# Optimization experiments

Measured on AMD Instinct MI355X. Metric: run time of the kernel, lower is better.

The kernel has to match this reference:

```python
import jax, jax.numpy as jnp
import numpy as np

ALPHA = 2.0  # init kwarg alpha


def _edt(mask):
    """Exact Euclidean distance from each pixel to the nearest False pixel.
    mask: (H, W) bool. Matches scipy.ndimage.distance_transform_edt(mask).
    Separable algorithm: 1D L1 pass along columns, then exact min over columns.
    """
    H, W = mask.shape
    INF = jnp.float32(H + W)
    g0 = jnp.where(mask, INF, 0.0).astype(jnp.float32)  # 0 at background pixels

    def step(carry, row):
        g = jnp.minimum(row, carry + 1.0)
        return g, g

    _, fwd = jax.lax.scan(step, jnp.full((W,), INF, jnp.float32), g0)
    _, bwd = jax.lax.scan(step, jnp.full((W,), INF, jnp.float32), fwd[::-1])
    g = bwd[::-1]  # (H, W): vertical distance to nearest bg in same column

    j = jnp.arange(W, dtype=jnp.float32)
    d2 = (j[:, None] - j[None, :]) ** 2  # (Wj, Wk)
    # dist2[i, j] = min_k g[i, k]^2 + (j - k)^2   -> exact squared EDT
    dist2 = jnp.min(g[:, None, :] ** 2 + d2[None, :, :], axis=-1)  # (H, W)
    return jnp.sqrt(dist2)


def _distance_field(img):
    """img: (N, H, W) float. Replicates LogHausdorffDTLoss.distance_field per slice."""

    def one(ch):
        mask = ch > 0.5
        valid = jnp.logical_and(mask.any(), ~mask.all())
        field = _edt(mask) + _edt(~mask)  # fg_dist + bg_dist
        return jnp.where(valid, field, 0.0)

    # sequential map keeps peak memory to one (H, W, W) intermediate at a time
    return jax.lax.map(one, img)


def setup_inputs() -> dict:
    key = jax.random.key(0)
    k1, k2, k3 = jax.random.split(key, 3)
    B, C, H, W = 8, 4, 256, 256
    preds_S = jax.random.normal(k1, (B, C, H, W), dtype=jnp.float32)
    preds_T = jax.random.normal(k2, (B, C, H, W), dtype=jnp.float32)
    target = jax.random.uniform(k3, (B, 1, H, W), dtype=jnp.float32)
    return {"preds_S": preds_S, "preds_T": preds_T, "target": target}


def reference(preds_S, preds_T, target):
    # shapes already match -> no interpolation; sigmoid=False, softmax=True, C>1
    C = preds_S.shape[1]
    p = jax.nn.softmax(preds_S, axis=1)

    # to_onehot_y=True: target is overwritten by onehot(argmax(teacher)) (detached)
    pT = jax.lax.stop_gradient(preds_T)
    labels = jnp.argmax(pT, axis=1)  # (B, H, W)
    tgt = jax.nn.one_hot(labels, C, axis=1, dtype=p.dtype)  # (B, C, H, W)

    # include_background=False: drop channel 0
    p = p[:, 1:]
    tgt = tgt[:, 1:]
    B, Cc, H, W = p.shape

    pred_dt = _distance_field(jax.lax.stop_gradient(p).reshape(-1, H, W)).reshape(B, Cc, H, W)
    tgt_dt = _distance_field(tgt.reshape(-1, H, W)).reshape(B, Cc, H, W)
    pred_dt = jax.lax.stop_gradient(pred_dt)
    tgt_dt = jax.lax.stop_gradient(tgt_dt)

    err = (p - tgt) ** 2
    dist = pred_dt ** ALPHA + tgt_dt ** ALPHA
    # per-channel means all cover B*H*W elements -> mean of means == global mean
    loss = jnp.mean(err * dist)
    return jnp.log(loss + 1.0)
```

## Files before the change

### kernel.cpp

```cpp
#include <hip/hip_runtime.h>
#include <math.h>

#define HWTOT 65536
#define WD 256
#define NSL 24

static constexpr size_t OFF_PART = 256;
static constexpr size_t OFF_MASK = 24832;
static constexpr size_t OFF_ERR  = OFF_MASK + (size_t)NSL * HWTOT;
static constexpr size_t OFF_BITS = OFF_ERR + (size_t)NSL * HWTOT * 2;
static constexpr size_t OFF_GC   = OFF_BITS + (size_t)2 * NSL * 8 * WD * 4;

__global__ __launch_bounds__(256) void k_mask(
    const float* __restrict__ pS, const float* __restrict__ pT,
    unsigned char* __restrict__ mask, _Float16* __restrict__ err)
{
    int blk = blockIdx.x;
    int b   = blk >> 8;
    int hw  = (blk & 255) * 256 + threadIdx.x;

    const float* ps = pS + (size_t)b * 4 * HWTOT + hw;
    float s0 = ps[0], s1 = ps[HWTOT], s2 = ps[2 * HWTOT], s3 = ps[3 * HWTOT];
    float mx = fmaxf(fmaxf(s0, s1), fmaxf(s2, s3));
    float e0 = expf(s0 - mx), e1 = expf(s1 - mx), e2 = expf(s2 - mx), e3 = expf(s3 - mx);
    float inv = 1.0f / (e0 + e1 + e2 + e3);

    const float* pt = pT + (size_t)b * 4 * HWTOT + hw;
    float t0 = pt[0], t1 = pt[HWTOT], t2 = pt[2 * HWTOT], t3 = pt[3 * HWTOT];
    int lab = 0; float bm = t0;
    if (t1 > bm) { bm = t1; lab = 1; }
    if (t2 > bm) { bm = t2; lab = 2; }
    if (t3 > bm) { bm = t3; lab = 3; }

    float pv[3] = { e1 * inv, e2 * inv, e3 * inv };
    #pragma unroll
    for (int cc = 0; cc < 3; ++cc) {
        int sl = b * 3 + cc;
        bool mp = pv[cc] > 0.5f;
        bool mt = (lab == cc + 1);
        mask[(size_t)sl * HWTOT + hw] = (unsigned char)((mp ? 1 : 0) | (mt ? 2 : 0));
        float tcv = mt ? 1.0f : 0.0f;
        float ev = (pv[cc] - tcv) * (pv[cc] - tcv);
        err[(size_t)sl * HWTOT + hw] = (_Float16)ev;
    }
}

__global__ __launch_bounds__(256) void k_pack(
    const unsigned char* __restrict__ mask, unsigned* __restrict__ bits)
{
    int s = blockIdx.x;
    int k = blockIdx.y;
    int w = threadIdx.x;
    const unsigned char* m = mask + (size_t)s * HWTOT + k * 32 * WD + w;

    unsigned vp = 0, vt = 0;
    #pragma unroll
    for (int i = 0; i < 32; ++i) {
        unsigned v = m[i * WD];
        vp |= (v & 1u) << i;
        vt |= ((v >> 1) & 1u) << i;
    }
    bits[((size_t)(0 * NSL + s) * 8 + k) * WD + w] = vp;
    bits[((size_t)(1 * NSL + s) * 8 + k) * WD + w] = vt;
}

__device__ __forceinline__ void vgc_field(
    const unsigned Y[8], bool valid, int kk, int w,
    unsigned short* __restrict__ gout)
{
    unsigned wk = 0;
    #pragma unroll
    for (int j = 0; j < 8; ++j) if (j == kk) wk = Y[j];

    int ls = -1000, lc = -1000;
    #pragma unroll
    for (int j = 0; j < 8; ++j) {
        if (j < kk) {
            unsigned z = Y[j], zc = ~Y[j];
            ls = z  ? (32 * j + 31 - __clz(z))  : ls;
            lc = zc ? (32 * j + 31 - __clz(zc)) : lc;
        }
    }
    unsigned dupk[16];
    #pragma unroll
    for (int r = 0; r < 32; ++r) {
        int h = 32 * kk + r;
        int b = (wk >> r) & 1;
        int du = min(h - (b ? lc : ls), 512);
        if (r & 1) dupk[r >> 1] |= (unsigned)du << 16;
        else       dupk[r >> 1]  = (unsigned)du;
        ls = b ? h : ls;
        lc = b ? lc : h;
    }
    int ns = 100000, nc = 100000;
    #pragma unroll
    for (int j = 7; j >= 0; --j) {
        if (j > kk) {
            unsigned z = Y[j], zc = ~Y[j];
            ns = z  ? (32 * j + (__ffs(z)  - 1)) : ns;
            nc = zc ? (32 * j + (__ffs(zc) - 1)) : nc;
        }
    }
    #pragma unroll
    for (int r = 31; r >= 0; --r) {
        int h = 32 * kk + r;
        int b = (wk >> r) & 1;
        int dd = min((b ? nc : ns) - h, 512);
        unsigned pk = dupk[r >> 1];
        int du = (r & 1) ? (int)(pk >> 16) : (int)(pk & 0xffffu);
        int gcv = min(du, dd);
        gcv = valid ? gcv : 0;
        gout[h * WD + w] = (unsigned short)gcv;
        ns = b ? h : ns;
        nc = b ? nc : h;
    }
}

__global__ __launch_bounds__(256) void k_vgc(
    const unsigned* __restrict__ bits, unsigned short* __restrict__ gc)
{
    int s  = blockIdx.x;
    int kk = blockIdx.y;
    int w  = threadIdx.x;

    unsigned YP[8], YT[8];
    #pragma unroll
    for (int j = 0; j < 8; ++j) {
        YP[j] = bits[((size_t)(0 * NSL + s) * 8 + j) * WD + w];
        YT[j] = bits[((size_t)(1 * NSL + s) * 8 + j) * WD + w];
    }

    unsigned oP = 0, aP = 0xFFFFFFFFu, oT = 0, aT = 0xFFFFFFFFu;
    #pragma unroll
    for (int j = 0; j < 8; ++j) {
        oP |= YP[j]; aP &= YP[j];
        oT |= YT[j]; aT &= YT[j];
    }
    #pragma unroll
    for (int i = 1; i < 64; i <<= 1) {
        oP |= __shfl_xor(oP, i); aP &= __shfl_xor(aP, i);
        oT |= __shfl_xor(oT, i); aT &= __shfl_xor(aT, i);
    }
    __shared__ unsigned rb[4][4];
    if ((w & 63) == 0) {
        int wv = w >> 6;
        rb[wv][0] = oP; rb[wv][1] = aP; rb[wv][2] = oT; rb[wv][3] = aT;
    }
    __syncthreads();
    oP = rb[0][0] | rb[1][0] | rb[2][0] | rb[3][0];
    aP = rb[0][1] & rb[1][1] & rb[2][1] & rb[3][1];
    oT = rb[0][2] | rb[1][2] | rb[2][2] | rb[3][2];
    aT = rb[0][3] & rb[1][3] & rb[2][3] & rb[3][3];
    bool validP = (oP != 0u) && (aP != 0xFFFFFFFFu);
    bool validT = (oT != 0u) && (aT != 0xFFFFFFFFu);

    vgc_field(YP, validP, kk, w, gc + (size_t)(0 * NSL + s) * HWTOT);
    vgc_field(YT, validT, kk, w, gc + (size_t)(1 * NSL + s) * HWTOT);
}

__global__ __launch_bounds__(256) void k_row(
    const _Float16* __restrict__ err, const unsigned* __restrict__ bits,
    const unsigned short* __restrict__ gcArr, float* __restrict__ partials)
{
    int h  = blockIdx.x;
    int s  = blockIdx.y;
    int jo = threadIdx.x;

    __shared__ float4 g2[768];
    __shared__ float  wred[4];

    size_t rbase = (size_t)s * HWTOT + h * WD + jo;
    int gcP = gcArr[rbase];
    int gcT = gcArr[(size_t)NSL * HWTOT + rbase];
    unsigned wP = bits[((size_t)(0 * NSL + s) * 8 + (h >> 5)) * WD + jo];
    unsigned wT = bits[((size_t)(1 * NSL + s) * 8 + (h >> 5)) * WD + jo];
    bool selP = (wP >> (h & 31)) & 1;
    bool selT = (wT >> (h & 31)) & 1;

    float fP = (float)(gcP * gcP);
    float fT = (float)(gcT * gcT);
    g2[256 + jo] = make_float4(selP ? fP : 0.0f, selP ? 0.0f : fP,
                               selT ? fT : 0.0f, selT ? 0.0f : fT);
    float4 inf4 = make_float4(1e30f, 1e30f, 1e30f, 1e30f);
    g2[jo] = inf4;
    g2[512 + jo] = inf4;

    int R = min(max(gcP, gcT), 256);
    #pragma unroll
    for (int i = 1; i < 64; i <<= 1) R = max(R, __shfl_xor(R, i));

    float m1 = fP;
    float m2 = fT;
    __syncthreads();

    for (int dd = 1; dd < R; ++dd) {
        float4 L  = g2[256 + jo - dd];
        float4 Rv = g2[256 + jo + dd];
        float d2 = (float)(dd * dd);
        float c1 = fminf(selP ? L.x : L.y, selP ? Rv.x : Rv.y);
        float c2 = fminf(selT ? L.z : L.w, selT ? Rv.z : Rv.w);
        m1 = fminf(m1, c1 + d2);
        m2 = fminf(m2, c2 + d2);
    }

    float contrib = (float)err[rbase] * (m1 + m2);

    #pragma unroll
    for (int off = 32; off > 0; off >>= 1) contrib += __shfl_down(contrib, off);
    if ((jo & 63) == 0) wred[jo >> 6] = contrib;
    __syncthreads();
    if (jo == 0) partials[s * 256 + h] = wred[0] + wred[1] + wred[2] + wred[3];
}

__global__ __launch_bounds__(256) void k_final(
    const float* __restrict__ partials, float* __restrict__ out)
{
    __shared__ double red[256];
    int t = threadIdx.x;
    double acc = 0.0;
    for (int i = t; i < NSL * 256; i += 256) acc += (double)partials[i];
    red[t] = acc;
    __syncthreads();
    for (int off = 128; off > 0; off >>= 1) {
        if (t < off) red[t] += red[t + off];
        __syncthreads();
    }
    if (t == 0) {
        double loss = red[0] / (double)((size_t)NSL * HWTOT);
        out[0] = (float)log(loss + 1.0);
    }
}

extern "C" void kernel_launch(void* const* d_in, const int* in_sizes, int n_in,
                              void* d_out, int out_size, void* d_ws, size_t ws_size,
                              hipStream_t stream)
{
    const float* pS = (const float*)d_in[0];
    const float* pT = (const float*)d_in[1];
    float* out = (float*)d_out;

    char* ws = (char*)d_ws;
    float*          parts = (float*)(ws + OFF_PART);
    unsigned char*  mask  = (unsigned char*)(ws + OFF_MASK);
    _Float16*       err   = (_Float16*)(ws + OFF_ERR);
    unsigned*       bits  = (unsigned*)(ws + OFF_BITS);
    unsigned short* gc    = (unsigned short*)(ws + OFF_GC);

    k_mask <<<dim3(2048),     dim3(256), 0, stream>>>(pS, pT, mask, err);
    k_pack <<<dim3(NSL, 8),   dim3(256), 0, stream>>>(mask, bits);
    k_vgc  <<<dim3(NSL, 8),   dim3(256), 0, stream>>>(bits, gc);
    k_row  <<<dim3(256, NSL), dim3(256), 0, stream>>>(err, bits, gc, parts);
    k_final<<<dim3(1),        dim3(256), 0, stream>>>(parts, out);
}
```

Baseline: 105.4 us.

## Fuse vertical pass, row min pass and final reduction into one kernel

Merges the column-distance, per-row horizontal min and final reduction kernels into one kernel. Column distances are kept in LDS instead of written to global memory, and a last-block atomic counter performs the final log reduction. This removes two launches and the global gc round-trip. In exchange the row pass goes from 6144 blocks to 192, with each block iterating 32 rows serially under barriers, which reduces parallelism.

```diff
diff --git a/kernel.cpp b/kernel.cpp
--- a/kernel.cpp
+++ b/kernel.cpp
@@ -4,12 +4,13 @@
 #define HWTOT 65536
 #define WD 256
 #define NSL 24
-
+#define NBLK (NSL * 8)
+
+static constexpr size_t OFF_DONE = 0;
 static constexpr size_t OFF_PART = 256;
 static constexpr size_t OFF_MASK = 24832;
 static constexpr size_t OFF_ERR  = OFF_MASK + (size_t)NSL * HWTOT;
 static constexpr size_t OFF_BITS = OFF_ERR + (size_t)NSL * HWTOT * 2;
-static constexpr size_t OFF_GC   = OFF_BITS + (size_t)2 * NSL * 8 * WD * 4;
 
 __global__ __launch_bounds__(256) void k_mask(
     const float* __restrict__ pS, const float* __restrict__ pT,
@@ -46,7 +47,8 @@
 }
 
 __global__ __launch_bounds__(256) void k_pack(
-    const unsigned char* __restrict__ mask, unsigned* __restrict__ bits)
+    const unsigned char* __restrict__ mask, unsigned* __restrict__ bits,
+    unsigned* __restrict__ done)
 {
     int s = blockIdx.x;
     int k = blockIdx.y;
@@ -62,9 +64,11 @@
     }
     bits[((size_t)(0 * NSL + s) * 8 + k) * WD + w] = vp;
     bits[((size_t)(1 * NSL + s) * 8 + k) * WD + w] = vt;
-}
-
-__device__ __forceinline__ void vgc_field(
+
+    if (s == 0 && k == 0 && w == 0) *done = 0;
+}
+
+__device__ __forceinline__ void vgc_field_lds(
     const unsigned Y[8], bool valid, int kk, int w,
     unsigned short* __restrict__ gout)
 {
@@ -110,26 +114,36 @@
         int du = (r & 1) ? (int)(pk >> 16) : (int)(pk & 0xffffu);
         int gcv = min(du, dd);
         gcv = valid ? gcv : 0;
-        gout[h * WD + w] = (unsigned short)gcv;
+        gout[r * WD + w] = (unsigned short)gcv;
         ns = b ? h : ns;
         nc = b ? nc : h;
     }
 }
 
-__global__ __launch_bounds__(256) void k_vgc(
-    const unsigned* __restrict__ bits, unsigned short* __restrict__ gc)
-{
-    int s  = blockIdx.x;
-    int kk = blockIdx.y;
-    int w  = threadIdx.x;
+__global__ __launch_bounds__(256) void k_fused(
+    const _Float16* __restrict__ err, const unsigned* __restrict__ bits,
+    float* __restrict__ partials, unsigned* __restrict__ done,
+    float* __restrict__ out)
+{
+    int s   = blockIdx.x;
+    int kk  = blockIdx.y;
+    int jo  = threadIdx.x;
+    int bid = s * 8 + kk;
+
+    __shared__ float4         g2[768];
+    __shared__ unsigned short gcP_l[32 * WD];
+    __shared__ unsigned short gcT_l[32 * WD];
+    __shared__ unsigned       rb[4][4];
+    __shared__ float          wred[4];
+    __shared__ int            amLast;
+    __shared__ double         dred[256];
 
     unsigned YP[8], YT[8];
     #pragma unroll
     for (int j = 0; j < 8; ++j) {
-        YP[j] = bits[((size_t)(0 * NSL + s) * 8 + j) * WD + w];
-        YT[j] = bits[((size_t)(1 * NSL + s) * 8 + j) * WD + w];
-    }
-
+        YP[j] = bits[((size_t)(0 * NSL + s) * 8 + j) * WD + jo];
+        YT[j] = bits[((size_t)(1 * NSL + s) * 8 + j) * WD + jo];
+    }
     unsigned oP = 0, aP = 0xFFFFFFFFu, oT = 0, aT = 0xFFFFFFFFu;
     #pragma unroll
     for (int j = 0; j < 8; ++j) {
@@ -141,9 +155,8 @@
         oP |= __shfl_xor(oP, i); aP &= __shfl_xor(aP, i);
         oT |= __shfl_xor(oT, i); aT &= __shfl_xor(aT, i);
     }
-    __shared__ unsigned rb[4][4];
-    if ((w & 63) == 0) {
-        int wv = w >> 6;
+    if ((jo & 63) == 0) {
+        int wv = jo >> 6;
         rb[wv][0] = oP; rb[wv][1] = aP; rb[wv][2] = oT; rb[wv][3] = aT;
     }
     __syncthreads();
@@ -154,80 +167,80 @@
     bool validP = (oP != 0u) && (aP != 0xFFFFFFFFu);
     bool validT = (oT != 0u) && (aT != 0xFFFFFFFFu);
 
-    vgc_field(YP, validP, kk, w, gc + (size_t)(0 * NSL + s) * HWTOT);
-    vgc_field(YT, validT, kk, w, gc + (size_t)(1 * NSL + s) * HWTOT);
-}
-
-__global__ __launch_bounds__(256) void k_row(
-    const _Float16* __restrict__ err, const unsigned* __restrict__ bits,
-    const unsigned short* __restrict__ gcArr, float* __restrict__ partials)
-{
-    int h  = blockIdx.x;
-    int s  = blockIdx.y;
-    int jo = threadIdx.x;
-
-    __shared__ float4 g2[768];
-    __shared__ float  wred[4];
-
-    size_t rbase = (size_t)s * HWTOT + h * WD + jo;
-    int gcP = gcArr[rbase];
-    int gcT = gcArr[(size_t)NSL * HWTOT + rbase];
-    unsigned wP = bits[((size_t)(0 * NSL + s) * 8 + (h >> 5)) * WD + jo];
-    unsigned wT = bits[((size_t)(1 * NSL + s) * 8 + (h >> 5)) * WD + jo];
-    bool selP = (wP >> (h & 31)) & 1;
-    bool selT = (wT >> (h & 31)) & 1;
-
-    float fP = (float)(gcP * gcP);
-    float fT = (float)(gcT * gcT);
-    g2[256 + jo] = make_float4(selP ? fP : 0.0f, selP ? 0.0f : fP,
-                               selT ? fT : 0.0f, selT ? 0.0f : fT);
+    vgc_field_lds(YP, validP, kk, jo, gcP_l);
+    vgc_field_lds(YT, validT, kk, jo, gcT_l);
+
+    unsigned wkP = 0, wkT = 0;
+    #pragma unroll
+    for (int j = 0; j < 8; ++j) if (j == kk) { wkP = YP[j]; wkT = YT[j]; }
+
     float4 inf4 = make_float4(1e30f, 1e30f, 1e30f, 1e30f);
     g2[jo] = inf4;
     g2[512 + jo] = inf4;
-
-    int R = min(max(gcP, gcT), 256);
-    #pragma unroll
-    for (int i = 1; i < 64; i <<= 1) R = max(R, __shfl_xor(R, i));
-
-    float m1 = fP;
-    float m2 = fT;
-    __syncthreads();
-
-    for (int dd = 1; dd < R; ++dd) {
-        float4 L  = g2[256 + jo - dd];
-        float4 Rv = g2[256 + jo + dd];
-        float d2 = (float)(dd * dd);
-        float c1 = fminf(selP ? L.x : L.y, selP ? Rv.x : Rv.y);
-        float c2 = fminf(selT ? L.z : L.w, selT ? Rv.z : Rv.w);
-        m1 = fminf(m1, c1 + d2);
-        m2 = fminf(m2, c2 + d2);
-    }
-
-    float contrib = (float)err[rbase] * (m1 + m2);
-
-    #pragma unroll
-    for (int off = 32; off > 0; off >>= 1) contrib += __shfl_down(contrib, off);
-    if ((jo & 63) == 0) wred[jo >> 6] = contrib;
-    __syncthreads();
-    if (jo == 0) partials[s * 256 + h] = wred[0] + wred[1] + wred[2] + wred[3];
-}
-
-__global__ __launch_bounds__(256) void k_final(
-    const float* __restrict__ partials, float* __restrict__ out)
-{
-    __shared__ double red[256];
-    int t = threadIdx.x;
-    double acc = 0.0;
-    for (int i = t; i < NSL * 256; i += 256) acc += (double)partials[i];
-    red[t] = acc;
-    __syncthreads();
-    for (int off = 128; off > 0; off >>= 1) {
-        if (t < off) red[t] += red[t + off];
+    __syncthreads();
+
+    float accum = 0.0f;
+    for (int r = 0; r < 32; ++r) {
+        int h = kk * 32 + r;
+        int gcP = gcP_l[r * WD + jo];
+        int gcT = gcT_l[r * WD + jo];
+        bool selP = (wkP >> r) & 1;
+        bool selT = (wkT >> r) & 1;
+
+        float fP = (float)(gcP * gcP);
+        float fT = (float)(gcT * gcT);
+        g2[256 + jo] = make_float4(selP ? fP : 0.0f, selP ? 0.0f : fP,
+                                   selT ? fT : 0.0f, selT ? 0.0f : fT);
+
+        int R = min(max(gcP, gcT), 256);
+        #pragma unroll
+        for (int i = 1; i < 64; i <<= 1) R = max(R, __shfl_xor(R, i));
+
+        float m1 = fP;
+        float m2 = fT;
         __syncthreads();
-    }
-    if (t == 0) {
-        double loss = red[0] / (double)((size_t)NSL * HWTOT);
-        out[0] = (float)log(loss + 1.0);
+
+        for (int dd = 1; dd < R; ++dd) {
+            float4 L  = g2[256 + jo - dd];
+            float4 Rv = g2[256 + jo + dd];
+            float d2 = (float)(dd * dd);
+            float c1 = fminf(selP ? L.x : L.y, selP ? Rv.x : Rv.y);
+            float c2 = fminf(selT ? L.z : L.w, selT ? Rv.z : Rv.w);
+            m1 = fminf(m1, c1 + d2);
+            m2 = fminf(m2, c2 + d2);
+        }
+
+        float e = (float)err[(size_t)s * HWTOT + h * WD + jo];
+        accum += e * (m1 + m2);
+        __syncthreads();
+    }
+
+    #pragma unroll
+    for (int off = 32; off > 0; off >>= 1) accum += __shfl_down(accum, off);
+    if ((jo & 63) == 0) wred[jo >> 6] = accum;
+    __syncthreads();
+    if (jo == 0) {
+        float total = wred[0] + wred[1] + wred[2] + wred[3];
+        atomicExch(&partials[bid], total);
+        __threadfence();
+        unsigned prev = atomicAdd(done, 1u);
+        amLast = (prev == NBLK - 1) ? 1 : 0;
+    }
+    __syncthreads();
+
+    if (amLast) {
+        int t = threadIdx.x;
+        double acc = (t < NBLK) ? (double)atomicAdd(&partials[t], 0.0f) : 0.0;
+        dred[t] = acc;
+        __syncthreads();
+        for (int off = 128; off > 0; off >>= 1) {
+            if (t < off) dred[t] += dred[t + off];
+            __syncthreads();
+        }
+        if (t == 0) {
+            double loss = dred[0] / (double)((size_t)NSL * HWTOT);
+            out[0] = (float)log(loss + 1.0);
+        }
     }
 }
 
@@ -240,15 +253,13 @@
     float* out = (float*)d_out;
 
     char* ws = (char*)d_ws;
+    unsigned*       done  = (unsigned*)(ws + OFF_DONE);
     float*          parts = (float*)(ws + OFF_PART);
     unsigned char*  mask  = (unsigned char*)(ws + OFF_MASK);
     _Float16*       err   = (_Float16*)(ws + OFF_ERR);
     unsigned*       bits  = (unsigned*)(ws + OFF_BITS);
-    unsigned short* gc    = (unsigned short*)(ws + OFF_GC);
-
-    k_mask <<<dim3(2048),     dim3(256), 0, stream>>>(pS, pT, mask, err);
-    k_pack <<<dim3(NSL, 8),   dim3(256), 0, stream>>>(mask, bits);
-    k_vgc  <<<dim3(NSL, 8),   dim3(256), 0, stream>>>(bits, gc);
-    k_row  <<<dim3(256, NSL), dim3(256), 0, stream>>>(err, bits, gc, parts);
-    k_final<<<dim3(1),        dim3(256), 0, stream>>>(parts, out);
-}
+
+    k_mask <<<dim3(2048),   dim3(256), 0, stream>>>(pS, pT, mask, err);
+    k_pack <<<dim3(NSL, 8), dim3(256), 0, stream>>>(mask, bits, done);
+    k_fused<<<dim3(NSL, 8), dim3(256), 0, stream>>>(err, bits, parts, done, out);
+}
```

Measured after the change: 169.6 us. 60.9% more time.
